# Performance work log

Measured on AMD Instinct MI355X. Metric: run time of the kernel, lower is better.

## Reference

```python
import jax, jax.numpy as jnp
import numpy as np

C = 4  # n_features_per_level
RES = [128, 256, 512, 1024]  # base_resolution=128, per_level_scale=2, n_levels=4


def grid_sample(grid, pts):
    """Bilinear grid_sample, align_corners=False, zero padding.
    grid: (B, C, H, W); pts: (B, N, 2) with pts[...,0]=x (width), pts[...,1]=y (height).
    Returns (B, C, N)."""
    B, Cc, H, W = grid.shape
    fx = (pts[..., 0] + 1.0) * 0.5 * W - 0.5
    fy = (pts[..., 1] + 1.0) * 0.5 * H - 0.5
    x0 = jnp.floor(fx)
    y0 = jnp.floor(fy)
    wx = (fx - x0)[:, None, :]
    wy = (fy - y0)[:, None, :]
    x0 = x0.astype(jnp.int32)
    y0 = y0.astype(jnp.int32)

    def corner(xi, yi):
        valid = ((xi >= 0) & (xi < W) & (yi >= 0) & (yi < H)).astype(grid.dtype)
        xc = jnp.clip(xi, 0, W - 1)
        yc = jnp.clip(yi, 0, H - 1)
        vals = jax.vmap(lambda g, yy, xx: g[:, yy, xx])(grid, yc, xc)  # (B, C, N)
        return vals * valid[:, None, :]

    v00 = corner(x0, y0)
    v10 = corner(x0 + 1, y0)
    v01 = corner(x0, y0 + 1)
    v11 = corner(x0 + 1, y0 + 1)
    return (v00 * (1 - wx) * (1 - wy) + v10 * wx * (1 - wy)
            + v01 * (1 - wx) * wy + v11 * wx * wy)


def _flat(f):
    # (3, C, N) -> (N, 3*C), matching torch out.reshape(3*C, N).T
    return f.reshape(3 * f.shape[1], f.shape[2]).T


def _forward(x, triplanes, trilines):
    x2 = x * 2.0 - 1.0  # map [0,1] -> [-1,1]
    # plane projections: (xz), (yx), (zy)
    x_pl = jnp.stack([
        jnp.stack([x2[:, 0], x2[:, 2]], -1),
        jnp.stack([x2[:, 1], x2[:, 0]], -1),
        jnp.stack([x2[:, 2], x2[:, 1]], -1)], 0)  # (3, N, 2)
    x_li = jnp.stack([x2[:, 0], x2[:, 1], x2[:, 2]], 0)
    x_li = jnp.stack([x_li, jnp.zeros_like(x_li)], -1)  # (3, N, 2)
    feats = []
    for tp, tl in zip(triplanes, trilines):
        f = _flat(grid_sample(tp, x_pl)) * _flat(grid_sample(tl, x_li))  # (N, 3C)
        feats.append(f)
    return jnp.concatenate(feats, -1)  # (N, 3*C*n_levels)


def setup_inputs() -> dict:
    key = jax.random.key(0)
    ks = jax.random.split(key, 9)
    N = 1 << 20
    d = {"x": jax.random.uniform(ks[0], (N, 3), jnp.float32)}
    for i, r in enumerate(RES):
        d[f"triplane_{i}"] = jax.random.normal(ks[1 + i], (3, C, r, r), jnp.float32)
        d[f"triline_{i}"] = jax.random.normal(ks[5 + i], (3, C, r, 1), jnp.float32)
    return d


def reference(x, triplane_0, triplane_1, triplane_2, triplane_3,
              triline_0, triline_1, triline_2, triline_3):
    triplanes = [triplane_0, triplane_1, triplane_2, triplane_3]
    trilines = [triline_0, triline_1, triline_2, triline_3]
    return _forward(x, triplanes, trilines)
```

## Files before the change

### kernel.cpp

```cpp
#include <hip/hip_runtime.h>
#include <cstdint>


typedef float f32x4 __attribute__((ext_vector_type(4)));

static constexpr int Q1_0 = 0;
static constexpr int Q1_1 = 199692;
static constexpr int Q1_2 = 992280;
static constexpr int Q1_3 = 4150308;
static constexpr int Q1_END = 16757808;
static constexpr int S1_OFF = Q1_END * 4;
static constexpr size_t WS1_NEED = ((size_t)S1_OFF + 48) * sizeof(float);

static constexpr int QE0 = 199692;
static constexpr int QE1 = 992280;
static constexpr int QE2 = 4150308;
static constexpr int L3T = 3145728;
static constexpr int T2_TOTAL = QE2 + L3T;
static constexpr int S2_OFF = (QE2 + L3T) * 4;
static constexpr size_t WS2_NEED = (size_t)(S2_OFF + 48) * sizeof(float);

__global__ __launch_bounds__(256) void prep_quads_all(
        const float* __restrict__ tp0, const float* __restrict__ tp1,
        const float* __restrict__ tp2, const float* __restrict__ tp3,
        const float* __restrict__ tl0, const float* __restrict__ tl1,
        const float* __restrict__ tl2, const float* __restrict__ tl3,
        float* __restrict__ ws) {
    int t = blockIdx.x * 256 + threadIdx.x;
    if (t < 48) {
        int ll = t / 12, rem = t % 12, pp = rem >> 2, cc = rem & 3;
        const float* tl = (ll == 0) ? tl0 : (ll == 1) ? tl1 : (ll == 2) ? tl2 : tl3;
        int r = 128 << ll;
        const float* row = tl + (size_t)((pp << 2) + cc) * r;
        int y0 = (r >> 1) - 1;
        ws[S1_OFF + t] = 0.5f * row[y0] + 0.5f * row[y0 + 1];
    }
    if (t >= Q1_END) return;
    const float* src; int lvl, base;
    if (t < Q1_1)      { src = tp0; lvl = 0; base = Q1_0; }
    else if (t < Q1_2) { src = tp1; lvl = 1; base = Q1_1; }
    else if (t < Q1_3) { src = tp2; lvl = 2; base = Q1_2; }
    else               { src = tp3; lvl = 3; base = Q1_3; }
    int lt = t - base;
    int q = lt >> 2, s = lt & 3;
    int r = 128 << lvl, R = r + 1, rr_shift = 2 * (7 + lvl);
    int RR = R * R;
    int p   = q / RR;
    int rem = q - p * RR;
    int yq  = rem / R;
    int xq  = rem - yq * R;
    int tx = xq - 1 + (s & 1);
    int ty = yq - 1 + (s >> 1);
    float4 o = {0.f, 0.f, 0.f, 0.f};
    if ((unsigned)tx < (unsigned)r && (unsigned)ty < (unsigned)r) {
        const float* sp = src + ((size_t)(p << 2) << rr_shift) + (size_t)ty * r + tx;
        o.x = sp[0];
        o.y = sp[(size_t)1 << rr_shift];
        o.z = sp[(size_t)2 << rr_shift];
        o.w = sp[(size_t)3 << rr_shift];
    }
    reinterpret_cast<float4*>(ws)[t] = o;
}

struct BilinW {
    int i00, i10, i01, i11;
    float w00, w10, w01, w11;
};

__device__ __forceinline__ BilinW bilin_weights(int r, float u, float v) {
    float fr = (float)r;
    float fx = (u + 1.0f) * 0.5f * fr - 0.5f;
    float fy = (v + 1.0f) * 0.5f * fr - 0.5f;
    float x0f = floorf(fx), y0f = floorf(fy);
    float wx = fx - x0f, wy = fy - y0f;
    int x0 = (int)x0f, y0 = (int)y0f;
    int x1 = x0 + 1, y1 = y0 + 1;
    float vx0 = ((unsigned)x0 < (unsigned)r) ? 1.0f : 0.0f;
    float vx1 = ((unsigned)x1 < (unsigned)r) ? 1.0f : 0.0f;
    float vy0 = ((unsigned)y0 < (unsigned)r) ? 1.0f : 0.0f;
    float vy1 = ((unsigned)y1 < (unsigned)r) ? 1.0f : 0.0f;
    int x0c = min(max(x0, 0), r - 1), x1c = min(max(x1, 0), r - 1);
    int y0c = min(max(y0, 0), r - 1), y1c = min(max(y1, 0), r - 1);
    BilinW b;
    b.i00 = y0c * r + x0c; b.i10 = y0c * r + x1c;
    b.i01 = y1c * r + x0c; b.i11 = y1c * r + x1c;
    b.w00 = (1.0f - wx) * (1.0f - wy) * vx0 * vy0;
    b.w10 = wx * (1.0f - wy) * vx1 * vy0;
    b.w01 = (1.0f - wx) * wy * vx0 * vy1;
    b.w11 = wx * wy * vx1 * vy1;
    return b;
}

__device__ __forceinline__ float line_w(float t) {
    float fx = (t + 1.0f) * 0.5f - 0.5f;
    float x0f = floorf(fx);
    float wx = fx - x0f;
    int x0 = (int)x0f;
    float w = 0.0f;
    if (x0 == 0) w += 1.0f - wx;
    if (x0 == -1) w += wx;
    return w;
}

template <bool VEC4OUT>
__global__ __launch_bounds__(256) void tri12q(const float* __restrict__ x,
                                              const f32x4* __restrict__ ws4,
                                              const float* __restrict__ S,
                                              float* __restrict__ out, int N) {
    int gid = blockIdx.x * 256 + threadIdx.x;
    int n = gid / 12;
    int k = gid - n * 12;
    if (n >= N) return;
    float ax = x[n * 3 + 0] * 2.0f - 1.0f;
    float ay = x[n * 3 + 1] * 2.0f - 1.0f;
    float az = x[n * 3 + 2] * 2.0f - 1.0f;
    int l = k / 3;
    int p = k - l * 3;
    float u = (p == 0) ? ax : (p == 1) ? ay : az;
    float v = (p == 0) ? az : (p == 1) ? ax : ay;
    float lw = line_w(u);
    f32x4 s = reinterpret_cast<const f32x4*>(S)[k];

    int r = 128 << l, R = r + 1;
    float fr = (float)r;
    float fx = (u + 1.0f) * 0.5f * fr - 0.5f;
    float fy = (v + 1.0f) * 0.5f * fr - 0.5f;
    float x0f = floorf(fx), y0f = floorf(fy);
    float wx = fx - x0f, wy = fy - y0f;
    int ix = (int)x0f + 1;
    int iy = (int)y0f + 1;
    ix = min(max(ix, 0), R - 1);
    iy = min(max(iy, 0), R - 1);
    int qbase = (l == 0) ? Q1_0 : (l == 1) ? Q1_1 : (l == 2) ? Q1_2 : Q1_3;
    const f32x4* Q = ws4 + qbase + (size_t)((p * R + iy) * R + ix) * 4;
    f32x4 q0 = Q[0], q1 = Q[1], q2 = Q[2], q3 = Q[3];
    float w00 = (1.0f - wx) * (1.0f - wy), w10 = wx * (1.0f - wy);
    float w01 = (1.0f - wx) * wy,          w11 = wx * wy;
    f32x4 o = q0 * w00 + q1 * w10 + q2 * w01 + q3 * w11;
    o = o * (s * lw);

    if (VEC4OUT) {
        __builtin_nontemporal_store(o, reinterpret_cast<f32x4*>(out) + gid);
    } else {
        size_t base = (size_t)gid * 4;
        out[base + 0] = o.x; out[base + 1] = o.y;
        out[base + 2] = o.z; out[base + 3] = o.w;
    }
}

__global__ __launch_bounds__(256) void prep_all(
        const float* __restrict__ tp0, const float* __restrict__ tp1,
        const float* __restrict__ tp2, const float* __restrict__ tp3,
        const float* __restrict__ tl0, const float* __restrict__ tl1,
        const float* __restrict__ tl2, const float* __restrict__ tl3,
        float* __restrict__ ws) {
    int t = blockIdx.x * 256 + threadIdx.x;
    if (t < 48) {
        int ll = t / 12, rem = t % 12, pp = rem >> 2, cc = rem & 3;
        const float* tl = (ll == 0) ? tl0 : (ll == 1) ? tl1 : (ll == 2) ? tl2 : tl3;
        int r = 128 << ll;
        const float* row = tl + (size_t)((pp << 2) + cc) * r;
        int y0 = (r >> 1) - 1;
        ws[S2_OFF + t] = 0.5f * row[y0] + 0.5f * row[y0 + 1];
    }
    if (t >= T2_TOTAL) return;
    float4* ws4 = reinterpret_cast<float4*>(ws);
    if (t < QE2) {
        const float* src; int lvl, base;
        if (t < QE0)      { src = tp0; lvl = 0; base = 0; }
        else if (t < QE1) { src = tp1; lvl = 1; base = QE0; }
        else              { src = tp2; lvl = 2; base = QE1; }
        int lt = t - base;
        int q = lt >> 2, s = lt & 3;
        int r = 128 << lvl, R = r + 1, rr_shift = 2 * (7 + lvl);
        int RR = R * R;
        int p   = q / RR;
        int rem = q - p * RR;
        int yq  = rem / R;
        int xq  = rem - yq * R;
        int tx = xq - 1 + (s & 1);
        int ty = yq - 1 + (s >> 1);
        float4 o = {0.f, 0.f, 0.f, 0.f};
        if ((unsigned)tx < (unsigned)r && (unsigned)ty < (unsigned)r) {
            const float* sp = src + ((size_t)(p << 2) << rr_shift) + (size_t)ty * r + tx;
            o.x = sp[0];
            o.y = sp[(size_t)1 << rr_shift];
            o.z = sp[(size_t)2 << rr_shift];
            o.w = sp[(size_t)3 << rr_shift];
        }
        ws4[t] = o;
    } else {
        int t2 = t - QE2;
        int p  = t2 >> 20;
        int yx = t2 & 0xFFFFF;
        const float* sp = tp3 + ((size_t)(p << 2) << 20) + yx;
        float4 o;
        o.x = sp[0];
        o.y = sp[(size_t)1 << 20];
        o.z = sp[(size_t)2 << 20];
        o.w = sp[(size_t)3 << 20];
        ws4[t] = o;
    }
}

template <bool VEC4OUT>
__global__ __launch_bounds__(256) void tri12(const float* __restrict__ x,
                                             const f32x4* __restrict__ ws4,
                                             const float* __restrict__ S,
                                             float* __restrict__ out, int N) {
    int gid = blockIdx.x * 256 + threadIdx.x;
    int n = gid / 12;
    int k = gid - n * 12;
    if (n >= N) return;
    float ax = x[n * 3 + 0] * 2.0f - 1.0f;
    float ay = x[n * 3 + 1] * 2.0f - 1.0f;
    float az = x[n * 3 + 2] * 2.0f - 1.0f;
    int l = k / 3;
    int p = k - l * 3;
    float u = (p == 0) ? ax : (p == 1) ? ay : az;
    float v = (p == 0) ? az : (p == 1) ? ax : ay;
    float lw = line_w(u);
    f32x4 s = reinterpret_cast<const f32x4*>(S)[k];

    f32x4 o;
    if (l < 3) {
        int r = 128 << l, R = r + 1;
        float fr = (float)r;
        float fx = (u + 1.0f) * 0.5f * fr - 0.5f;
        float fy = (v + 1.0f) * 0.5f * fr - 0.5f;
        float x0f = floorf(fx), y0f = floorf(fy);
        float wx = fx - x0f, wy = fy - y0f;
        int ix = (int)x0f + 1;
        int iy = (int)y0f + 1;
        ix = min(max(ix, 0), R - 1);
        iy = min(max(iy, 0), R - 1);
        int qbase = (l == 0) ? 0 : (l == 1) ? QE0 : QE1;
        const f32x4* Q = ws4 + qbase + (size_t)((p * R + iy) * R + ix) * 4;
        f32x4 q0 = Q[0], q1 = Q[1], q2 = Q[2], q3 = Q[3];
        float w00 = (1.0f - wx) * (1.0f - wy), w10 = wx * (1.0f - wy);
        float w01 = (1.0f - wx) * wy,          w11 = wx * wy;
        o = q0 * w00 + q1 * w10 + q2 * w01 + q3 * w11;
    } else {
        BilinW b = bilin_weights(1024, u, v);
        const f32x4* G = ws4 + QE2 + (size_t)p * 1048576;
        f32x4 g0 = G[b.i00], g1 = G[b.i10], g2 = G[b.i01], g3 = G[b.i11];
        o = g0 * b.w00 + g1 * b.w10 + g2 * b.w01 + g3 * b.w11;
    }
    o = o * (s * lw);

    if (VEC4OUT) {
        __builtin_nontemporal_store(o, reinterpret_cast<f32x4*>(out) + gid);
    } else {
        size_t base = (size_t)gid * 4;
        out[base + 0] = o.x; out[base + 1] = o.y;
        out[base + 2] = o.z; out[base + 3] = o.w;
    }
}

__global__ __launch_bounds__(256) void tri_direct(
        const float* __restrict__ x,
        const float* __restrict__ tp0, const float* __restrict__ tp1,
        const float* __restrict__ tp2, const float* __restrict__ tp3,
        const float* __restrict__ tl0, const float* __restrict__ tl1,
        const float* __restrict__ tl2, const float* __restrict__ tl3,
        float* __restrict__ out, int N) {
    int n = blockIdx.x * blockDim.x + threadIdx.x;
    if (n >= N) return;
    float ax = x[n * 3 + 0] * 2.0f - 1.0f;
    float ay = x[n * 3 + 1] * 2.0f - 1.0f;
    float az = x[n * 3 + 2] * 2.0f - 1.0f;
    const float U[3] = {ax, ay, az};
    const float V[3] = {az, ax, ay};
    const float LW[3] = {line_w(ax), line_w(ay), line_w(az)};
    const float* TP[4] = {tp0, tp1, tp2, tp3};
    const float* TL[4] = {tl0, tl1, tl2, tl3};

#pragma unroll
    for (int l = 0; l < 4; ++l) {
        const int r = 128 << l;
        const int rr = r * r;
        const int y0 = (r >> 1) - 1;
#pragma unroll
        for (int p = 0; p < 3; ++p) {
            const float* G = TP[l] + (size_t)(p * 4) * rr;
            BilinW b = bilin_weights(r, U[p], V[p]);
            const float w = LW[p];
#pragma unroll
            for (int c = 0; c < 4; ++c) {
                const float* Gc = G + (size_t)c * rr;
                float acc = Gc[b.i00] * b.w00 + Gc[b.i10] * b.w10 +
                            Gc[b.i01] * b.w01 + Gc[b.i11] * b.w11;
                const float* row = TL[l] + (size_t)((p << 2) + c) * r;
                float s = 0.5f * row[y0] + 0.5f * row[y0 + 1];
                out[(size_t)n * 48 + l * 12 + p * 4 + c] = acc * (s * w);
            }
        }
    }
}

extern "C" void kernel_launch(void* const* d_in, const int* in_sizes, int n_in,
                              void* d_out, int out_size, void* d_ws, size_t ws_size,
                              hipStream_t stream) {
    const float* x = (const float*)d_in[0];
    const float* tp[4];
    const float* tl[4];
    bool interleaved = (n_in >= 9) && (in_sizes[2] == 1536);
    for (int l = 0; l < 4; ++l) {
        if (interleaved) {
            tp[l] = (const float*)d_in[1 + 2 * l];
            tl[l] = (const float*)d_in[2 + 2 * l];
        } else {
            tp[l] = (const float*)d_in[1 + l];
            tl[l] = (const float*)d_in[5 + l];
        }
    }
    int N = in_sizes[0] / 3;
    float* out = (float*)d_out;
    bool out16 = (((uintptr_t)d_out & 15u) == 0);

    if (ws_size >= WS1_NEED && (((uintptr_t)d_ws & 63u) == 0)) {
        float* ws = (float*)d_ws;
        int prep_grid = (Q1_END + 255) / 256;
        prep_quads_all<<<prep_grid, 256, 0, stream>>>(
            tp[0], tp[1], tp[2], tp[3], tl[0], tl[1], tl[2], tl[3], ws);
        long long total = 12LL * N;
        int grid = (int)((total + 255) / 256);
        if (out16) {
            tri12q<true><<<grid, 256, 0, stream>>>(
                x, (const f32x4*)ws, ws + S1_OFF, out, N);
        } else {
            tri12q<false><<<grid, 256, 0, stream>>>(
                x, (const f32x4*)ws, ws + S1_OFF, out, N);
        }
    } else if (ws_size >= WS2_NEED && (((uintptr_t)d_ws & 63u) == 0)) {
        float* ws = (float*)d_ws;
        int prep_grid = (T2_TOTAL + 255) / 256;
        prep_all<<<prep_grid, 256, 0, stream>>>(
            tp[0], tp[1], tp[2], tp[3], tl[0], tl[1], tl[2], tl[3], ws);
        long long total = 12LL * N;
        int grid = (int)((total + 255) / 256);
        if (out16) {
            tri12<true><<<grid, 256, 0, stream>>>(
                x, (const f32x4*)ws, ws + S2_OFF, out, N);
        } else {
            tri12<false><<<grid, 256, 0, stream>>>(
                x, (const f32x4*)ws, ws + S2_OFF, out, N);
        }
    } else {
        int grid = (N + 255) / 256;
        tri_direct<<<grid, 256, 0, stream>>>(
            x, tp[0], tp[1], tp[2], tp[3], tl[0], tl[1], tl[2], tl[3], out, N);
    }
}
```

Baseline: 536.3 us.

## Sort points by Morton key before gathering quad-packed triplane features

Adds a counting sort of input points into 64^3 Morton-order buckets (histogram, two-level scan, atomic scatter), then runs the 12-way gather kernel over the sorted points and writes each result back to its original output slot. The aim is to give the gathers into the large quad-expanded plane tables spatial locality, so they hit in L2/MALL instead of missing randomly. It also remaps block IDs across 8 groups, likely to spread work across XCDs. The cost is five extra kernel launches plus a memset, atomics on the histogram, and output writes that are now scattered rather than sequential. The old non-quad fallback path is removed.

```diff
diff --git a/kernel.cpp b/kernel.cpp
--- a/kernel.cpp
+++ b/kernel.cpp
@@ -12,13 +12,10 @@
 static constexpr int S1_OFF = Q1_END * 4;
 static constexpr size_t WS1_NEED = ((size_t)S1_OFF + 48) * sizeof(float);
 
-static constexpr int QE0 = 199692;
-static constexpr int QE1 = 992280;
-static constexpr int QE2 = 4150308;
-static constexpr int L3T = 3145728;
-static constexpr int T2_TOTAL = QE2 + L3T;
-static constexpr int S2_OFF = (QE2 + L3T) * 4;
-static constexpr size_t WS2_NEED = (size_t)(S2_OFF + 48) * sizeof(float);
+static constexpr int NBUCK  = 262144;
+static constexpr int HIST_F = S1_OFF + 64;
+static constexpr int BSUM_F = HIST_F + NBUCK;
+static constexpr int XS_F   = BSUM_F + 1024;
 
 __global__ __launch_bounds__(256) void prep_quads_all(
         const float* __restrict__ tp0, const float* __restrict__ tp1,
@@ -102,6 +99,143 @@
     return w;
 }
 
+__device__ __forceinline__ unsigned spread3(unsigned v) {
+    v &= 63u;
+    v = (v | (v << 8)) & 0x00F00Fu;
+    v = (v | (v << 4)) & 0x0C30C3u;
+    v = (v | (v << 2)) & 0x249249u;
+    return v;
+}
+
+__device__ __forceinline__ unsigned mkey(float x, float y, float z) {
+    int qx = min(63, max(0, (int)(x * 64.0f)));
+    int qy = min(63, max(0, (int)(y * 64.0f)));
+    int qz = min(63, max(0, (int)(z * 64.0f)));
+    return spread3(qx) | (spread3(qy) << 1) | (spread3(qz) << 2);
+}
+
+__global__ __launch_bounds__(256) void hist_pts(const float* __restrict__ x,
+                                                unsigned* __restrict__ hist, int N) {
+    int n = blockIdx.x * 256 + threadIdx.x;
+    if (n >= N) return;
+    unsigned k = mkey(x[n * 3 + 0], x[n * 3 + 1], x[n * 3 + 2]);
+    atomicAdd(&hist[k], 1u);
+}
+
+__global__ __launch_bounds__(256) void reduce_hist(const unsigned* __restrict__ hist,
+                                                   unsigned* __restrict__ bsum) {
+    __shared__ unsigned lds[256];
+    int t = threadIdx.x;
+    lds[t] = hist[blockIdx.x * 256 + t];
+    __syncthreads();
+    for (int off = 128; off > 0; off >>= 1) {
+        if (t < off) lds[t] += lds[t + off];
+        __syncthreads();
+    }
+    if (t == 0) bsum[blockIdx.x] = lds[0];
+}
+
+__global__ __launch_bounds__(1024) void scan_bsum(unsigned* __restrict__ bsum) {
+    __shared__ unsigned tmp[1024];
+    int t = threadIdx.x;
+    unsigned v = bsum[t];
+    tmp[t] = v;
+    __syncthreads();
+    for (int off = 1; off < 1024; off <<= 1) {
+        unsigned add = (t >= off) ? tmp[t - off] : 0u;
+        __syncthreads();
+        tmp[t] += add;
+        __syncthreads();
+    }
+    bsum[t] = tmp[t] - v;
+}
+
+__global__ __launch_bounds__(256) void scan_hist(unsigned* __restrict__ hist,
+                                                 const unsigned* __restrict__ bsum) {
+    __shared__ unsigned tmp[256];
+    int t = threadIdx.x;
+    int base = blockIdx.x * 256;
+    unsigned v = hist[base + t];
+    tmp[t] = v;
+    __syncthreads();
+    for (int off = 1; off < 256; off <<= 1) {
+        unsigned add = (t >= off) ? tmp[t - off] : 0u;
+        __syncthreads();
+        tmp[t] += add;
+        __syncthreads();
+    }
+    hist[base + t] = tmp[t] - v + bsum[blockIdx.x];
+}
+
+__global__ __launch_bounds__(256) void scatter_pts(const float* __restrict__ x,
+                                                   unsigned* __restrict__ offs,
+                                                   float4* __restrict__ xs, int N) {
+    int n = blockIdx.x * 256 + threadIdx.x;
+    if (n >= N) return;
+    float xv = x[n * 3 + 0], yv = x[n * 3 + 1], zv = x[n * 3 + 2];
+    unsigned k = mkey(xv, yv, zv);
+    unsigned pos = atomicAdd(&offs[k], 1u);
+    float4 v;
+    v.x = xv * 2.0f - 1.0f;
+    v.y = yv * 2.0f - 1.0f;
+    v.z = zv * 2.0f - 1.0f;
+    v.w = __int_as_float(n);
+    xs[pos] = v;
+}
+
+template <bool VEC4OUT>
+__global__ __launch_bounds__(256) void tri12s(const float4* __restrict__ xs,
+                                              const f32x4* __restrict__ ws4,
+                                              const float* __restrict__ S,
+                                              float* __restrict__ out, int N) {
+    int bid = blockIdx.x;
+    int nb = gridDim.x;
+    if ((nb & 7) == 0) {
+        int cpx = nb >> 3;
+        bid = (bid & 7) * cpx + (bid >> 3);
+    }
+    int gid = bid * 256 + threadIdx.x;
+    int m = gid / 12;
+    int k = gid - m * 12;
+    if (m >= N) return;
+    float4 xv = xs[m];
+    float ax = xv.x, ay = xv.y, az = xv.z;
+    int n = __float_as_int(xv.w);
+    int l = k / 3;
+    int p = k - l * 3;
+    float u = (p == 0) ? ax : (p == 1) ? ay : az;
+    float v = (p == 0) ? az : (p == 1) ? ax : ay;
+    float lw = line_w(u);
+    f32x4 s = reinterpret_cast<const f32x4*>(S)[k];
+
+    int r = 128 << l, R = r + 1;
+    float fr = (float)r;
+    float fx = (u + 1.0f) * 0.5f * fr - 0.5f;
+    float fy = (v + 1.0f) * 0.5f * fr - 0.5f;
+    float x0f = floorf(fx), y0f = floorf(fy);
+    float wx = fx - x0f, wy = fy - y0f;
+    int ix = (int)x0f + 1;
+    int iy = (int)y0f + 1;
+    ix = min(max(ix, 0), R - 1);
+    iy = min(max(iy, 0), R - 1);
+    int qbase = (l == 0) ? Q1_0 : (l == 1) ? Q1_1 : (l == 2) ? Q1_2 : Q1_3;
+    const f32x4* Q = ws4 + qbase + (size_t)((p * R + iy) * R + ix) * 4;
+    f32x4 q0 = Q[0], q1 = Q[1], q2 = Q[2], q3 = Q[3];
+    float w00 = (1.0f - wx) * (1.0f - wy), w10 = wx * (1.0f - wy);
+    float w01 = (1.0f - wx) * wy,          w11 = wx * wy;
+    f32x4 o = q0 * w00 + q1 * w10 + q2 * w01 + q3 * w11;
+    o = o * (s * lw);
+
+    size_t oslot = (size_t)n * 12 + k;
+    if (VEC4OUT) {
+        __builtin_nontemporal_store(o, reinterpret_cast<f32x4*>(out) + oslot);
+    } else {
+        size_t base = oslot * 4;
+        out[base + 0] = o.x; out[base + 1] = o.y;
+        out[base + 2] = o.z; out[base + 3] = o.w;
+    }
+}
+
 template <bool VEC4OUT>
 __global__ __launch_bounds__(256) void tri12q(const float* __restrict__ x,
                                               const f32x4* __restrict__ ws4,
@@ -137,115 +271,6 @@
     float w00 = (1.0f - wx) * (1.0f - wy), w10 = wx * (1.0f - wy);
     float w01 = (1.0f - wx) * wy,          w11 = wx * wy;
     f32x4 o = q0 * w00 + q1 * w10 + q2 * w01 + q3 * w11;
-    o = o * (s * lw);
-
-    if (VEC4OUT) {
-        __builtin_nontemporal_store(o, reinterpret_cast<f32x4*>(out) + gid);
-    } else {
-        size_t base = (size_t)gid * 4;
-        out[base + 0] = o.x; out[base + 1] = o.y;
-        out[base + 2] = o.z; out[base + 3] = o.w;
-    }
-}
-
-__global__ __launch_bounds__(256) void prep_all(
-        const float* __restrict__ tp0, const float* __restrict__ tp1,
-        const float* __restrict__ tp2, const float* __restrict__ tp3,
-        const float* __restrict__ tl0, const float* __restrict__ tl1,
-        const float* __restrict__ tl2, const float* __restrict__ tl3,
-        float* __restrict__ ws) {
-    int t = blockIdx.x * 256 + threadIdx.x;
-    if (t < 48) {
-        int ll = t / 12, rem = t % 12, pp = rem >> 2, cc = rem & 3;
-        const float* tl = (ll == 0) ? tl0 : (ll == 1) ? tl1 : (ll == 2) ? tl2 : tl3;
-        int r = 128 << ll;
-        const float* row = tl + (size_t)((pp << 2) + cc) * r;
-        int y0 = (r >> 1) - 1;
-        ws[S2_OFF + t] = 0.5f * row[y0] + 0.5f * row[y0 + 1];
-    }
-    if (t >= T2_TOTAL) return;
-    float4* ws4 = reinterpret_cast<float4*>(ws);
-    if (t < QE2) {
-        const float* src; int lvl, base;
-        if (t < QE0)      { src = tp0; lvl = 0; base = 0; }
-        else if (t < QE1) { src = tp1; lvl = 1; base = QE0; }
-        else              { src = tp2; lvl = 2; base = QE1; }
-        int lt = t - base;
-        int q = lt >> 2, s = lt & 3;
-        int r = 128 << lvl, R = r + 1, rr_shift = 2 * (7 + lvl);
-        int RR = R * R;
-        int p   = q / RR;
-        int rem = q - p * RR;
-        int yq  = rem / R;
-        int xq  = rem - yq * R;
-        int tx = xq - 1 + (s & 1);
-        int ty = yq - 1 + (s >> 1);
-        float4 o = {0.f, 0.f, 0.f, 0.f};
-        if ((unsigned)tx < (unsigned)r && (unsigned)ty < (unsigned)r) {
-            const float* sp = src + ((size_t)(p << 2) << rr_shift) + (size_t)ty * r + tx;
-            o.x = sp[0];
-            o.y = sp[(size_t)1 << rr_shift];
-            o.z = sp[(size_t)2 << rr_shift];
-            o.w = sp[(size_t)3 << rr_shift];
-        }
-        ws4[t] = o;
-    } else {
-        int t2 = t - QE2;
-        int p  = t2 >> 20;
-        int yx = t2 & 0xFFFFF;
-        const float* sp = tp3 + ((size_t)(p << 2) << 20) + yx;
-        float4 o;
-        o.x = sp[0];
-        o.y = sp[(size_t)1 << 20];
-        o.z = sp[(size_t)2 << 20];
-        o.w = sp[(size_t)3 << 20];
-        ws4[t] = o;
-    }
-}
-
-template <bool VEC4OUT>
-__global__ __launch_bounds__(256) void tri12(const float* __restrict__ x,
-                                             const f32x4* __restrict__ ws4,
-                                             const float* __restrict__ S,
-                                             float* __restrict__ out, int N) {
-    int gid = blockIdx.x * 256 + threadIdx.x;
-    int n = gid / 12;
-    int k = gid - n * 12;
-    if (n >= N) return;
-    float ax = x[n * 3 + 0] * 2.0f - 1.0f;
-    float ay = x[n * 3 + 1] * 2.0f - 1.0f;
-    float az = x[n * 3 + 2] * 2.0f - 1.0f;
-    int l = k / 3;
-    int p = k - l * 3;
-    float u = (p == 0) ? ax : (p == 1) ? ay : az;
-    float v = (p == 0) ? az : (p == 1) ? ax : ay;
-    float lw = line_w(u);
-    f32x4 s = reinterpret_cast<const f32x4*>(S)[k];
-
-    f32x4 o;
-    if (l < 3) {
-        int r = 128 << l, R = r + 1;
-        float fr = (float)r;
-        float fx = (u + 1.0f) * 0.5f * fr - 0.5f;
-        float fy = (v + 1.0f) * 0.5f * fr - 0.5f;
-        float x0f = floorf(fx), y0f = floorf(fy);
-        float wx = fx - x0f, wy = fy - y0f;
-        int ix = (int)x0f + 1;
-        int iy = (int)y0f + 1;
-        ix = min(max(ix, 0), R - 1);
-        iy = min(max(iy, 0), R - 1);
-        int qbase = (l == 0) ? 0 : (l == 1) ? QE0 : QE1;
-        const f32x4* Q = ws4 + qbase + (size_t)((p * R + iy) * R + ix) * 4;
-        f32x4 q0 = Q[0], q1 = Q[1], q2 = Q[2], q3 = Q[3];
-        float w00 = (1.0f - wx) * (1.0f - wy), w10 = wx * (1.0f - wy);
-        float w01 = (1.0f - wx) * wy,          w11 = wx * wy;
-        o = q0 * w00 + q1 * w10 + q2 * w01 + q3 * w11;
-    } else {
-        BilinW b = bilin_weights(1024, u, v);
-        const f32x4* G = ws4 + QE2 + (size_t)p * 1048576;
-        f32x4 g0 = G[b.i00], g1 = G[b.i10], g2 = G[b.i01], g3 = G[b.i11];
-        o = g0 * b.w00 + g1 * b.w10 + g2 * b.w01 + g3 * b.w11;
-    }
     o = o * (s * lw);
 
     if (VEC4OUT) {
@@ -317,11 +342,38 @@
     int N = in_sizes[0] / 3;
     float* out = (float*)d_out;
     bool out16 = (((uintptr_t)d_out & 15u) == 0);
-
-    if (ws_size >= WS1_NEED && (((uintptr_t)d_ws & 63u) == 0)) {
+    bool ws64 = (((uintptr_t)d_ws & 63u) == 0);
+
+    size_t need_sorted = ((size_t)XS_F + 4ull * (size_t)N) * sizeof(float);
+
+    if (ws_size >= need_sorted && ws64) {
         float* ws = (float*)d_ws;
-        int prep_grid = (Q1_END + 255) / 256;
-        prep_quads_all<<<prep_grid, 256, 0, stream>>>(
+        unsigned* hist = reinterpret_cast<unsigned*>(ws + HIST_F);
+        unsigned* bsum = reinterpret_cast<unsigned*>(ws + BSUM_F);
+        float4*   xs   = reinterpret_cast<float4*>(ws + XS_F);
+        int gN = (N + 255) / 256;
+
+        prep_quads_all<<<(Q1_END + 255) / 256, 256, 0, stream>>>(
+            tp[0], tp[1], tp[2], tp[3], tl[0], tl[1], tl[2], tl[3], ws);
+        hipMemsetAsync(hist, 0, (size_t)NBUCK * sizeof(unsigned), stream);
+        hist_pts<<<gN, 256, 0, stream>>>(x, hist, N);
+        reduce_hist<<<NBUCK / 256, 256, 0, stream>>>(hist, bsum);
+        scan_bsum<<<1, 1024, 0, stream>>>(bsum);
+        scan_hist<<<NBUCK / 256, 256, 0, stream>>>(hist, bsum);
+        scatter_pts<<<gN, 256, 0, stream>>>(x, hist, xs, N);
+
+        long long total = 12LL * N;
+        int grid = (int)((total + 255) / 256);
+        if (out16) {
+            tri12s<true><<<grid, 256, 0, stream>>>(
+                xs, (const f32x4*)ws, ws + S1_OFF, out, N);
+        } else {
+            tri12s<false><<<grid, 256, 0, stream>>>(
+                xs, (const f32x4*)ws, ws + S1_OFF, out, N);
+        }
+    } else if (ws_size >= WS1_NEED && ws64) {
+        float* ws = (float*)d_ws;
+        prep_quads_all<<<(Q1_END + 255) / 256, 256, 0, stream>>>(
             tp[0], tp[1], tp[2], tp[3], tl[0], tl[1], tl[2], tl[3], ws);
         long long total = 12LL * N;
         int grid = (int)((total + 255) / 256);
@@ -332,20 +384,6 @@
             tri12q<false><<<grid, 256, 0, stream>>>(
                 x, (const f32x4*)ws, ws + S1_OFF, out, N);
         }
-    } else if (ws_size >= WS2_NEED && (((uintptr_t)d_ws & 63u) == 0)) {
-        float* ws = (float*)d_ws;
-        int prep_grid = (T2_TOTAL + 255) / 256;
-        prep_all<<<prep_grid, 256, 0, stream>>>(
-            tp[0], tp[1], tp[2], tp[3], tl[0], tl[1], tl[2], tl[3], ws);
-        long long total = 12LL * N;
-        int grid = (int)((total + 255) / 256);
-        if (out16) {
-            tri12<true><<<grid, 256, 0, stream>>>(
-                x, (const f32x4*)ws, ws + S2_OFF, out, N);
-        } else {
-            tri12<false><<<grid, 256, 0, stream>>>(
-                x, (const f32x4*)ws, ws + S2_OFF, out, N);
-        }
     } else {
         int grid = (N + 255) / 256;
         tri_direct<<<grid, 256, 0, stream>>>(
```

After: 634.4 us. 18.3% more time.
